# Optimization experiments

Hardware: AMD Instinct MI355X
Metric: run time of the kernel (lower is better)

## Reference

```python
import jax, jax.numpy as jnp
import numpy as np


def setup_inputs() -> dict:
    key = jax.random.key(0)
    k1, k2, k3 = jax.random.split(key, 3)
    B, S, I, H = 32, 1024, 512, 1024
    x = jax.random.normal(k1, (B, S, I), dtype=jnp.float32)
    W_in = jax.random.normal(k2, (I, H), dtype=jnp.float32) * 0.1
    W_rec = jax.random.normal(k3, (H, H), dtype=jnp.float32) * 0.1
    bias = jnp.zeros((H,), dtype=jnp.float32)
    tau = jnp.ones((H,), dtype=jnp.float32) * 0.1
    return {"x": x, "W_in": W_in, "W_rec": W_rec, "bias": bias, "tau": tau}


def reference(x, W_in, W_rec, bias, tau):
    # x: [B, S, I]; liquid / CT-RNN cell with leaky integration.
    B = x.shape[0]
    H = W_rec.shape[0]
    DT = 0.05  # integration step used in the original module
    alpha = jnp.exp(-DT / tau)  # [H], constant across timesteps
    h0 = jnp.zeros((B, H), dtype=x.dtype)
    # Precompute input projection for all steps in one big GEMM: [B,S,H]
    h_in_all = jnp.einsum('bsi,ih->bsh', x, W_in)

    def step(h, h_in_t):
        h_total = jnp.tanh(h_in_t + h @ W_rec + bias)
        h_new = alpha * h + (1.0 - alpha) * h_total
        return h_new, h_new

    # scan over time: xs [S, B, H]
    h_last, outs = jax.lax.scan(step, h0, jnp.swapaxes(h_in_all, 0, 1))
    output = jnp.swapaxes(outs, 0, 1)  # [B, S, H]
    return output, h_last
```

## Files before the change

kernel.cpp:

```cpp
#include <hip/hip_runtime.h>
#include <cmath>

constexpr int B = 32, S = 1024, I = 512, H = 1024;
constexpr float DT = 0.05f;

__global__ __launch_bounds__(256) void gemm_in(const float* __restrict__ A,
                                               const float* __restrict__ Bw,
                                               float* __restrict__ C) {
    const int bx = blockIdx.x;
    const int nb = bx & 15;
    const int mb = bx >> 4;
    const int t  = threadIdx.x;
    const int tx = t & 15, ty = t >> 4;

    __shared__ __align__(16) float As[16][68];
    __shared__ __align__(16) float Bs[16][68];

    float acc[4][4] = {};
    const int row0 = mb * 64, col0 = nb * 64;

    for (int kt = 0; kt < I; kt += 16) {
        {
            const int m  = t >> 2;
            const int kq = (t & 3) * 4;
            const float4 a = *(const float4*)(A + (size_t)(row0 + m) * I + kt + kq);
            As[kq + 0][m] = a.x; As[kq + 1][m] = a.y;
            As[kq + 2][m] = a.z; As[kq + 3][m] = a.w;
            const int kk = t >> 4;
            const int n4 = (t & 15) * 4;
            *(float4*)&Bs[kk][n4] =
                *(const float4*)(Bw + (size_t)(kt + kk) * H + col0 + n4);
        }
        __syncthreads();
#pragma unroll
        for (int kk = 0; kk < 16; ++kk) {
            const float4 av = *(const float4*)&As[kk][ty * 4];
            const float4 bv = *(const float4*)&Bs[kk][tx * 4];
            const float ar[4] = {av.x, av.y, av.z, av.w};
            const float br[4] = {bv.x, bv.y, bv.z, bv.w};
#pragma unroll
            for (int i = 0; i < 4; ++i)
#pragma unroll
                for (int j = 0; j < 4; ++j) acc[i][j] += ar[i] * br[j];
        }
        __syncthreads();
    }
#pragma unroll
    for (int i = 0; i < 4; ++i) {
        float4 v = make_float4(acc[i][0], acc[i][1], acc[i][2], acc[i][3]);
        *(float4*)(C + (size_t)(row0 + ty * 4 + i) * H + col0 + tx * 4) = v;
    }
}

__device__ __forceinline__ void fma4(float4& acc, float sc, const float4 wv) {
    acc.x = fmaf(sc, wv.x, acc.x);
    acc.y = fmaf(sc, wv.y, acc.y);
    acc.z = fmaf(sc, wv.z, acc.z);
    acc.w = fmaf(sc, wv.w, acc.w);
}

__device__ __forceinline__ float lda(const float* p) {
    return __hip_atomic_load(p, __ATOMIC_RELAXED, __HIP_MEMORY_SCOPE_AGENT);
}
__device__ __forceinline__ void sta(float* p, float v) {
    __hip_atomic_store(p, v, __ATOMIC_RELAXED, __HIP_MEMORY_SCOPE_AGENT);
}

__global__ __launch_bounds__(256, 1) void scan_k(const float* __restrict__ Wrec,
                                                 const float* __restrict__ bias,
                                                 const float* __restrict__ tau,
                                                 float* __restrict__ out,
                                                 int* __restrict__ ws) {
    const int t    = threadIdx.x;
    const int bid  = blockIdx.x;
    const int rep  = bid & 7;
    const int slot = bid >> 3;
    const int b0   = rep * 4;
    const int c0   = slot * 32;

    __shared__ __align__(16) float h_lds[4 * 1152];
    __shared__ __align__(16) float part[32 * 132];

    int* const flags   = ws;
    int* const myflag  = flags + (((rep << 5) | (t >> 3)) << 5);
    int* const pubflag = flags + (((rep << 5) | slot) << 5);

    const int ks = t >> 3;
    const int cq = t & 7;
    const int cc = c0 + cq * 4;
    float4 wreg[32];
#pragma unroll
    for (int kk = 0; kk < 32; ++kk)
        wreg[kk] = *(const float4*)&Wrec[(size_t)(ks * 32 + kk) * H + cc];

    const int br = t >> 5, jc = t & 31;
    const int c  = c0 + jc;
    float al = 0.f, bi = 0.f;
    if (t < 128) { al = __expf(-DT / tau[c]); bi = bias[c]; }
    const size_t obase = (size_t)(b0 + br) * S * H + c;

    const int wa = 4 * t + (t >> 3) * 4;

    for (int s = 0; s < S; ++s) {
        if (s == 0) {
            const float4 z = make_float4(0.f, 0.f, 0.f, 0.f);
#pragma unroll
            for (int bb = 0; bb < 4; ++bb)
                *(float4*)&h_lds[bb * 1152 + wa] = z;
        } else {
            while (__hip_atomic_load(myflag, __ATOMIC_RELAXED,
                                     __HIP_MEMORY_SCOPE_AGENT) < s)
                __builtin_amdgcn_s_sleep(1);
            const float* src = out + (size_t)(s - 1) * H + 4 * t;
            const float* s0 = src + (size_t)(b0 + 0) * S * H;
            const float* s1 = src + (size_t)(b0 + 1) * S * H;
            const float* s2 = src + (size_t)(b0 + 2) * S * H;
            const float* s3 = src + (size_t)(b0 + 3) * S * H;
            const float4 v0 = make_float4(lda(s0), lda(s0+1), lda(s0+2), lda(s0+3));
            const float4 v1 = make_float4(lda(s1), lda(s1+1), lda(s1+2), lda(s1+3));
            const float4 v2 = make_float4(lda(s2), lda(s2+1), lda(s2+2), lda(s2+3));
            const float4 v3 = make_float4(lda(s3), lda(s3+1), lda(s3+2), lda(s3+3));
            *(float4*)&h_lds[0 * 1152 + wa] = v0;
            *(float4*)&h_lds[1 * 1152 + wa] = v1;
            *(float4*)&h_lds[2 * 1152 + wa] = v2;
            *(float4*)&h_lds[3 * 1152 + wa] = v3;
        }

        float hin = 0.f;
        if (t < 128) hin = out[obase + (size_t)s * H];

        __syncthreads();

        float4 a0 = make_float4(0.f, 0.f, 0.f, 0.f);
        float4 a1 = a0, a2 = a0, a3 = a0;
#pragma unroll
        for (int kq = 0; kq < 8; ++kq) {
            const int ha = ks * 36 + kq * 4;
            const float4 h0 = *(const float4*)&h_lds[ha];
            const float4 h1 = *(const float4*)&h_lds[1152 + ha];
            const float4 h2 = *(const float4*)&h_lds[2304 + ha];
            const float4 h3 = *(const float4*)&h_lds[3456 + ha];
            const float r0[4] = {h0.x, h0.y, h0.z, h0.w};
            const float r1[4] = {h1.x, h1.y, h1.z, h1.w};
            const float r2[4] = {h2.x, h2.y, h2.z, h2.w};
            const float r3[4] = {h3.x, h3.y, h3.z, h3.w};
#pragma unroll
            for (int j = 0; j < 4; ++j) {
                const float4 w = wreg[kq * 4 + j];
                fma4(a0, r0[j], w);
                fma4(a1, r1[j], w);
                fma4(a2, r2[j], w);
                fma4(a3, r3[j], w);
            }
        }
        {
            float* pp = &part[ks * 132 + cq * 4];
            *(float4*)(pp +  0) = a0;
            *(float4*)(pp + 32) = a1;
            *(float4*)(pp + 64) = a2;
            *(float4*)(pp + 96) = a3;
        }
        __syncthreads();

        if (t < 128) {
            float sum = 0.f;
#pragma unroll
            for (int q = 0; q < 32; ++q) sum += part[q * 132 + t];
            const float z  = hin + sum + bi;
            const float e2 = __expf(2.f * z);
            const float ht = 1.f - 2.f / (e2 + 1.f);
            const float hp = h_lds[br * 1152 + slot * 36 + jc];
            const float hn = al * hp + (1.f - al) * ht;
            sta(&out[obase + (size_t)s * H], hn);
            if (s == S - 1)
                out[(size_t)B * S * H + (size_t)(b0 + br) * H + c] = hn;
        }
        __syncthreads();
        if (t == 0)
            __hip_atomic_store(pubflag, s + 1, __ATOMIC_RELAXED,
                               __HIP_MEMORY_SCOPE_AGENT);
    }
}

extern "C" void kernel_launch(void* const* d_in, const int* in_sizes, int n_in,
                              void* d_out, int out_size, void* d_ws, size_t ws_size,
                              hipStream_t stream) {
    (void)in_sizes; (void)n_in; (void)out_size;
    const float* x    = (const float*)d_in[0];
    const float* W_in = (const float*)d_in[1];
    const float* Wrec = (const float*)d_in[2];
    const float* bs   = (const float*)d_in[3];
    const float* tu   = (const float*)d_in[4];
    float* outp = (float*)d_out;
    int*   bwsp = (int*)d_ws;

    size_t zb = 256 * 32 * sizeof(int);
    if (zb > ws_size) zb = ws_size;
    (void)hipMemsetAsync(d_ws, 0, zb, stream);

    gemm_in<<<dim3(512 * 16), dim3(256), 0, stream>>>(x, W_in, outp);

    void* kargs[5] = {(void*)&Wrec, (void*)&bs, (void*)&tu, (void*)&outp,
                      (void*)&bwsp};
    (void)hipLaunchCooperativeKernel((void*)scan_k, dim3(256), dim3(256), kargs,
                                     0, stream);
}
```

Baseline: 3.992 ms.

## Replace per-step flag barrier with canary-tagged data polling in recurrent scan

Drops the per-step publish flag and its trailing __syncthreads. Each block now overwrites its next-step output slot with a sentinel value, and consumers spin on 64-bit atomic loads of the hidden-state data itself until no sentinel remains. The next step's input projection is also prefetched one step ahead. This removes one barrier and a flag round trip per timestep. The risk is that a computed value bit-equal to the canary (2.0f) would cause a hang, though tanh-blended values stay below 1, and the load/store ordering depends on relaxed atomics.

New measurement: 3.436 ms. 13.9% less time.

```diff
diff --git a/kernel.cpp b/kernel.cpp
--- a/kernel.cpp
+++ b/kernel.cpp
@@ -3,6 +3,7 @@
 
 constexpr int B = 32, S = 1024, I = 512, H = 1024;
 constexpr float DT = 0.05f;
+constexpr unsigned CANARY = 0x40000000u;
 
 __global__ __launch_bounds__(256) void gemm_in(const float* __restrict__ A,
                                                const float* __restrict__ Bw,
@@ -59,11 +60,20 @@
     acc.w = fmaf(sc, wv.w, acc.w);
 }
 
-__device__ __forceinline__ float lda(const float* p) {
-    return __hip_atomic_load(p, __ATOMIC_RELAXED, __HIP_MEMORY_SCOPE_AGENT);
-}
 __device__ __forceinline__ void sta(float* p, float v) {
     __hip_atomic_store(p, v, __ATOMIC_RELAXED, __HIP_MEMORY_SCOPE_AGENT);
+}
+__device__ __forceinline__ unsigned long long ld2(const float* p) {
+    return __hip_atomic_load((const unsigned long long*)p, __ATOMIC_RELAXED,
+                             __HIP_MEMORY_SCOPE_AGENT);
+}
+__device__ __forceinline__ void stc(float* p, unsigned v) {
+    __hip_atomic_store((unsigned*)p, v, __ATOMIC_RELAXED,
+                       __HIP_MEMORY_SCOPE_AGENT);
+}
+__device__ __forceinline__ float uf(unsigned x) { return __uint_as_float(x); }
+__device__ __forceinline__ bool has_canary(unsigned long long q) {
+    return ((unsigned)q == CANARY) || ((unsigned)(q >> 32) == CANARY);
 }
 
 __global__ __launch_bounds__(256, 1) void scan_k(const float* __restrict__ Wrec,
@@ -101,35 +111,66 @@
 
     const int wa = 4 * t + (t >> 3) * 4;
 
+    float hinCur = 0.f;
+    if (t < 128) hinCur = out[obase];
+    __syncthreads();
+    if (t < 128) stc(&out[obase], CANARY);
+    __syncthreads();
+    if (t == 0)
+        __hip_atomic_store(pubflag, 1, __ATOMIC_RELAXED,
+                           __HIP_MEMORY_SCOPE_AGENT);
+
     for (int s = 0; s < S; ++s) {
+        float hinNext = 0.f;
+        if (t < 128 && s + 1 < S) hinNext = out[obase + (size_t)(s + 1) * H];
+
         if (s == 0) {
             const float4 z = make_float4(0.f, 0.f, 0.f, 0.f);
 #pragma unroll
             for (int bb = 0; bb < 4; ++bb)
                 *(float4*)&h_lds[bb * 1152 + wa] = z;
         } else {
-            while (__hip_atomic_load(myflag, __ATOMIC_RELAXED,
-                                     __HIP_MEMORY_SCOPE_AGENT) < s)
+            if (s == 1) {
+                while (__hip_atomic_load(myflag, __ATOMIC_RELAXED,
+                                         __HIP_MEMORY_SCOPE_AGENT) < 1)
+                    __builtin_amdgcn_s_sleep(1);
+            }
+            const float* src = out + (size_t)(s - 1) * H + 4 * t;
+            const float* p0 = src + (size_t)(b0 + 0) * S * H;
+            const float* p1 = src + (size_t)(b0 + 1) * S * H;
+            const float* p2 = src + (size_t)(b0 + 2) * S * H;
+            const float* p3 = src + (size_t)(b0 + 3) * S * H;
+            unsigned long long q0, q1, q2, q3, q4, q5, q6, q7;
+            for (;;) {
+                q0 = ld2(p0); q1 = ld2(p0 + 2);
+                q2 = ld2(p1); q3 = ld2(p1 + 2);
+                q4 = ld2(p2); q5 = ld2(p2 + 2);
+                q6 = ld2(p3); q7 = ld2(p3 + 2);
+                const bool bad = has_canary(q0) | has_canary(q1) |
+                                 has_canary(q2) | has_canary(q3) |
+                                 has_canary(q4) | has_canary(q5) |
+                                 has_canary(q6) | has_canary(q7);
+                if (!bad) break;
                 __builtin_amdgcn_s_sleep(1);
-            const float* src = out + (size_t)(s - 1) * H + 4 * t;
-            const float* s0 = src + (size_t)(b0 + 0) * S * H;
-            const float* s1 = src + (size_t)(b0 + 1) * S * H;
-            const float* s2 = src + (size_t)(b0 + 2) * S * H;
-            const float* s3 = src + (size_t)(b0 + 3) * S * H;
-            const float4 v0 = make_float4(lda(s0), lda(s0+1), lda(s0+2), lda(s0+3));
-            const float4 v1 = make_float4(lda(s1), lda(s1+1), lda(s1+2), lda(s1+3));
-            const float4 v2 = make_float4(lda(s2), lda(s2+1), lda(s2+2), lda(s2+3));
-            const float4 v3 = make_float4(lda(s3), lda(s3+1), lda(s3+2), lda(s3+3));
+            }
+            const float4 v0 = make_float4(uf((unsigned)q0), uf((unsigned)(q0 >> 32)),
+                                          uf((unsigned)q1), uf((unsigned)(q1 >> 32)));
+            const float4 v1 = make_float4(uf((unsigned)q2), uf((unsigned)(q2 >> 32)),
+                                          uf((unsigned)q3), uf((unsigned)(q3 >> 32)));
+            const float4 v2 = make_float4(uf((unsigned)q4), uf((unsigned)(q4 >> 32)),
+                                          uf((unsigned)q5), uf((unsigned)(q5 >> 32)));
+            const float4 v3 = make_float4(uf((unsigned)q6), uf((unsigned)(q6 >> 32)),
+                                          uf((unsigned)q7), uf((unsigned)(q7 >> 32)));
             *(float4*)&h_lds[0 * 1152 + wa] = v0;
             *(float4*)&h_lds[1 * 1152 + wa] = v1;
             *(float4*)&h_lds[2 * 1152 + wa] = v2;
             *(float4*)&h_lds[3 * 1152 + wa] = v3;
         }
 
-        float hin = 0.f;
-        if (t < 128) hin = out[obase + (size_t)s * H];
-
-        __syncthreads();
+        __syncthreads();
+
+        if (t < 128 && s + 1 < S)
+            stc(&out[obase + (size_t)(s + 1) * H], CANARY);
 
         float4 a0 = make_float4(0.f, 0.f, 0.f, 0.f);
         float4 a1 = a0, a2 = a0, a3 = a0;
@@ -166,7 +207,7 @@
             float sum = 0.f;
 #pragma unroll
             for (int q = 0; q < 32; ++q) sum += part[q * 132 + t];
-            const float z  = hin + sum + bi;
+            const float z  = hinCur + sum + bi;
             const float e2 = __expf(2.f * z);
             const float ht = 1.f - 2.f / (e2 + 1.f);
             const float hp = h_lds[br * 1152 + slot * 36 + jc];
@@ -175,10 +216,7 @@
             if (s == S - 1)
                 out[(size_t)B * S * H + (size_t)(b0 + br) * H + c] = hn;
         }
-        __syncthreads();
-        if (t == 0)
-            __hip_atomic_store(pubflag, s + 1, __ATOMIC_RELAXED,
-                               __HIP_MEMORY_SCOPE_AGENT);
+        hinCur = hinNext;
     }
 }
 
```
